# Kernel tuning notes

Hardware: AMD Instinct MI355X
Metric: run time of the kernel (lower is better)

The kernel has to match this reference:

```python
import jax, jax.numpy as jnp
import numpy as np

N = 30000   # fluid particles
E = 480000  # edges
F = 4       # fluidFeatures (in channels)
P = 8       # RBF basis size per dim (dims=[8], 1D)
LAYERS = [32, 64, 64, 2]


def hat_basis(x, n):
    # 'linear' RBF: hat functions on n evenly spaced centers in [-1, 1]
    centers = jnp.linspace(-1.0, 1.0, n, dtype=x.dtype)
    spacing = 2.0 / (n - 1)
    return jnp.maximum(0.0, 1.0 - jnp.abs(x[:, None] - centers[None, :]) / spacing)  # [E, n]


def rbf_conv(x, fi, fj, d, W, b, mask, n_nodes):
    # x: [N, Cin]; d: [E, 1] clamped; W: [P, Cin, Cout]; b: [Cout]
    phi = hat_basis(d[:, 0], W.shape[0])      # [E, P]
    xj = x[fj]                                 # gather source features [E, Cin]
    msg = jnp.zeros((xj.shape[0], W.shape[2]), dtype=x.dtype)
    for p in range(W.shape[0]):                # small fixed P=8 loop keeps memory O(E*Cout)
        msg = msg + phi[:, p, None] * (xj @ W[p])
    msg = jnp.where(mask[:, None], msg, 0.0)   # centerIgnore: drop self edges fi==fj
    out = jax.ops.segment_sum(msg, fi, num_segments=n_nodes)  # scatter-reduce to targets
    return out + b


def _xavier(key, shape_in, shape_out):
    lim = float(np.sqrt(6.0 / (shape_in + shape_out)))
    return jax.random.uniform(key, (shape_in, shape_out), jnp.float32, -lim, lim)


def setup_inputs() -> dict:
    key = jax.random.key(0)
    ks = jax.random.split(key, 16)
    fluidFeatures = jax.random.normal(ks[0], (N, F), jnp.float32)
    fi = jax.random.randint(ks[1], (E,), 0, N)
    fj = jax.random.randint(ks[2], (E,), 0, N)
    distances = jax.random.normal(ks[3], (E, 1), jnp.float32)
    # conv channels: 4->32, 64->64, 64->64, 64->2
    cio = [(F, 32), (2 * 32, 64), (64, 64), (64, 2)]
    inp = {"fluidFeatures": fluidFeatures, "fi": fi, "fj": fj, "distances": distances}
    for li, (ci, co) in enumerate(cio):
        inp[f"cW{li}"] = jax.random.normal(ks[4 + li], (P, ci, co), jnp.float32) * (1.0 / np.sqrt(P * ci))
        inp[f"cb{li}"] = jnp.zeros((co,), jnp.float32)
        inp[f"fW{li}"] = _xavier(ks[8 + li], ci, co)   # stored [in, out]
        inp[f"fb{li}"] = jnp.zeros((co,), jnp.float32)
    return inp


def reference(fluidFeatures, fi, fj, distances,
              cW0, cb0, fW0, fb0, cW1, cb1, fW1, fb1,
              cW2, cb2, fW2, fb2, cW3, cb3, fW3, fb3):
    n_nodes = fluidFeatures.shape[0]
    mask = fi != fj                     # centerIgnore (mask instead of filter: jit-safe)
    d = jnp.clip(distances, -1.0, 1.0)

    conv0 = rbf_conv(fluidFeatures, fi, fj, d, cW0, cb0, mask, n_nodes)  # [N, 32]
    lin0 = fluidFeatures @ fW0 + fb0                                      # [N, 32]
    ans = jnp.concatenate([lin0, conv0], axis=1)                          # [N, 64]

    # i = 1: features[0]=32 != features[1]=64 -> no residual
    ansc = jax.nn.relu(ans)
    ans = rbf_conv(ansc, fi, fj, d, cW1, cb1, mask, n_nodes) + (ansc @ fW1 + fb1)
    # i = 2: features[1]==features[2]==64 and shapes match -> residual
    ansc = jax.nn.relu(ans)
    ans = rbf_conv(ansc, fi, fj, d, cW2, cb2, mask, n_nodes) + (ansc @ fW2 + fb2) + ans
    # i = 3: 64 -> 2, no residual
    ansc = jax.nn.relu(ans)
    ans = rbf_conv(ansc, fi, fj, d, cW3, cb3, mask, n_nodes) + (ansc @ fW3 + fb3)

    return ans  # dim == 1 (dims=[8]) -> no /128
```

## Files before the change

kernel.cpp:

```cpp
#include <hip/hip_runtime.h>


#define CAP 48

typedef __attribute__((ext_vector_type(8))) short short8;
typedef __attribute__((ext_vector_type(4))) short short4v;
typedef __attribute__((ext_vector_type(4))) float f32x4;

__device__ __forceinline__ short bf16s(float f) {
  unsigned u = __float_as_uint(f);
  return (short)((u + 0x7FFF + ((u >> 16) & 1)) >> 16);
}
__device__ __forceinline__ float b2f(unsigned short s) {
  return __uint_as_float(((unsigned)s) << 16);
}

__global__ void fill_prep(const float* __restrict__ dist,
                          const int* __restrict__ fi, const int* __restrict__ fj,
                          int* __restrict__ cnt, int* __restrict__ jw, int nE,
                          const float* __restrict__ cW1, const float* __restrict__ fW1,
                          const float* __restrict__ cW2, const float* __restrict__ fW2,
                          short* __restrict__ wt1, short* __restrict__ wt2,
                          int fillBlocks) {
  if ((int)blockIdx.x < fillBlocks) {
    int e = blockIdx.x * blockDim.x + threadIdx.x;
    if (e >= nE) return;
    int i = fi[e], j = fj[e];
    if (i == j) return;
    float d = fminf(1.0f, fmaxf(-1.0f, dist[e]));
    float u = (d + 1.0f) * 3.5f;
    int p = min((int)u, 6);
    float w0 = 1.0f - (u - (float)p);
    int wq = (int)(w0 * 16383.0f + 0.5f);
    int pos = atomicAdd(&cnt[i], 1);
    if (pos < CAP)
      jw[(size_t)i * CAP + pos] = j | (p << 15) | (wq << 18);
  } else {
    int idx = ((int)blockIdx.x - fillBlocks) * blockDim.x + threadIdx.x;
    if (idx >= 2 * 576 * 64) return;
    int sel = idx / (576 * 64);
    int r = idx - sel * (576 * 64);
    int col = r >> 6, ch = r & 63;
    const float* cW = sel ? cW2 : cW1;
    const float* fW = sel ? fW2 : fW1;
    float v;
    if (col < 512) {
      int p = col >> 6, co = col & 63;
      v = cW[((size_t)p * 64 + ch) * 64 + co];
    } else {
      v = fW[(size_t)ch * 64 + (col - 512)];
    }
    (sel ? wt2 : wt1)[(size_t)col * 64 + ch] = bf16s(v);
  }
}

__global__ __launch_bounds__(256) void layer0_kernel(
    const float* __restrict__ X,
    const int* __restrict__ cnt, const int* __restrict__ jw,
    const float* __restrict__ cW0,
    const float* __restrict__ cb0,
    const float* __restrict__ fW0,
    const float* __restrict__ fb0,
    unsigned short* __restrict__ ansc0, int n) {
  __shared__ float sW[1024];
  __shared__ float sF[128];
  __shared__ float sB[64];
  __shared__ float sacc[4][32];
  for (int idx = threadIdx.x; idx < 1024; idx += 256) sW[idx] = cW0[idx];
  for (int idx = threadIdx.x; idx < 128; idx += 256) sF[idx] = fW0[idx];
  if (threadIdx.x < 32) sB[threadIdx.x] = cb0[threadIdx.x];
  else if (threadIdx.x < 64) sB[threadIdx.x] = fb0[threadIdx.x - 32];
  const int w = threadIdx.x >> 6;
  const int lane = threadIdx.x & 63;
  const int i = blockIdx.x * 4 + w;
  const bool valid = (i < n);
  if (valid && lane < 32) sacc[w][lane] = 0.0f;
  __syncthreads();
  if (valid && lane < min(cnt[i], CAP)) {
    int v = jw[(size_t)i * CAP + lane];
    int j = v & 0x7FFF;
    int p = (v >> 15) & 7;
    float w0 = (float)((unsigned)v >> 18) * (1.0f / 16383.0f);
    float w1 = 1.0f - w0;
    float4 x = *(const float4*)(X + (size_t)j * 4);
    atomicAdd(&sacc[w][p * 4 + 0], w0 * x.x);
    atomicAdd(&sacc[w][p * 4 + 1], w0 * x.y);
    atomicAdd(&sacc[w][p * 4 + 2], w0 * x.z);
    atomicAdd(&sacc[w][p * 4 + 3], w0 * x.w);
    atomicAdd(&sacc[w][(p + 1) * 4 + 0], w1 * x.x);
    atomicAdd(&sacc[w][(p + 1) * 4 + 1], w1 * x.y);
    atomicAdd(&sacc[w][(p + 1) * 4 + 2], w1 * x.z);
    atomicAdd(&sacc[w][(p + 1) * 4 + 3], w1 * x.w);
  }
  __syncthreads();
  if (!valid) return;
  const float4 xi = *(const float4*)(X + (size_t)i * 4);
  float v;
  if (lane < 32) {
    v = sB[32 + lane];
    v = fmaf(xi.x, sF[0 * 32 + lane], v);
    v = fmaf(xi.y, sF[1 * 32 + lane], v);
    v = fmaf(xi.z, sF[2 * 32 + lane], v);
    v = fmaf(xi.w, sF[3 * 32 + lane], v);
  } else {
    const int cc = lane - 32;
    v = sB[cc];
    #pragma unroll
    for (int k = 0; k < 32; ++k)
      v = fmaf(sacc[w][k], sW[k * 32 + cc], v);
  }
  ansc0[(size_t)i * 64 + lane] = (unsigned short)bf16s(fmaxf(v, 0.0f));
}

__global__ __launch_bounds__(256) void gemm_ul(
    const unsigned short* __restrict__ Xb,
    const short* __restrict__ WTul,
    unsigned short* __restrict__ UL, int n) {
  __shared__ short sUL[16 * 584];
  const int lane = threadIdx.x & 63;
  const int w = threadIdx.x >> 6;
  const int mrow = lane & 15;
  const int quad = lane >> 4;
  const int nodeBase = blockIdx.x * 16;
  const int bnode = min(nodeBase + mrow, n - 1);
  const unsigned short* bBase = Xb + (size_t)bnode * 64 + quad * 8;
  short8 b0 = *(const short8*)(bBase);
  short8 b1 = *(const short8*)(bBase + 32);
  #pragma unroll
  for (int t = 0; t < 9; ++t) {
    const int ct = w * 9 + t;
    const short* aBase = WTul + (size_t)(ct * 16 + mrow) * 64 + quad * 8;
    short8 a0 = *(const short8*)(aBase);
    short8 a1 = *(const short8*)(aBase + 32);
    f32x4 acc = {0, 0, 0, 0};
    acc = __builtin_amdgcn_mfma_f32_16x16x32_bf16(a0, b0, acc, 0, 0, 0);
    acc = __builtin_amdgcn_mfma_f32_16x16x32_bf16(a1, b1, acc, 0, 0, 0);
    short4v pk;
    #pragma unroll
    for (int reg = 0; reg < 4; ++reg) pk[reg] = bf16s(acc[reg]);
    *(short4v*)(sUL + mrow * 584 + ct * 16 + quad * 4) = pk;
  }
  __syncthreads();
  const int r = threadIdx.x >> 4;
  const int c0 = threadIdx.x & 15;
  if (nodeBase + r < n) {
    unsigned short* dst = UL + (size_t)(nodeBase + r) * 576;
    #pragma unroll
    for (int chunk = c0; chunk < 72; chunk += 16)
      *(short8*)(dst + chunk * 8) = *(const short8*)(sUL + r * 584 + chunk * 8);
  }
}

template <bool HAS_RES, bool STORE_ANS, bool COMPUTE_T>
__global__ __launch_bounds__(256) void conv_gather(
    const unsigned short* __restrict__ UL,
    const int* __restrict__ cnt, const int* __restrict__ jw,
    const float* __restrict__ cb, const float* __restrict__ fb,
    const float* __restrict__ resid,
    const float* __restrict__ cW3,
    float* __restrict__ T,
    float* __restrict__ outAns,
    unsigned short* __restrict__ outAnsc, int n) {
  const int lane = threadIdx.x & 63;
  const int half = lane >> 5;
  const int pl = lane & 31;
  const int i = (blockIdx.x * blockDim.x + threadIdx.x) >> 6;
  if (i >= n) return;
  int rec = jw[(size_t)i * CAP + (lane < CAP ? lane : 0)];
  const int m = min(cnt[i], CAP);
  const int mc = m - 1;
  const unsigned short* ULrow = UL + (size_t)i * 576;
  const unsigned Lraw = ((const unsigned*)(ULrow + 512))[pl];
  float rv0 = 0.0f, rv1 = 0.0f;
  if (HAS_RES) {
    float2 rv = *(const float2*)(resid + (size_t)i * 64 + 2 * pl);
    rv0 = rv.x; rv1 = rv.y;
  }
  float accLo = 0.0f, accHi = 0.0f;
  for (int q0 = 0; q0 < m; q0 += 16) {
    unsigned raw[16];
    float w0s[16];
    #pragma unroll
    for (int k = 0; k < 16; ++k) {
      int v = __builtin_amdgcn_readlane(rec, min(q0 + k, mc));
      int j = v & 0x7FFF;
      int p = (v >> 15) & 7;
      w0s[k] = (float)((unsigned)v >> 18) * (1.0f / 16383.0f);
      raw[k] = ((const unsigned*)(UL + (size_t)j * 576 + p * 64))[lane];
    }
    #pragma unroll
    for (int k = 0; k < 16; ++k) {
      bool ok = (q0 + k < m);
      float w = half ? (1.0f - w0s[k]) : w0s[k];
      w = ok ? w : 0.0f;
      accLo = fmaf(w, __uint_as_float(raw[k] << 16), accLo);
      accHi = fmaf(w, __uint_as_float(raw[k] & 0xFFFF0000u), accHi);
    }
  }
  accLo += __shfl_xor(accLo, 32, 64);
  accHi += __shfl_xor(accHi, 32, 64);
  if (half == 0) {
    const int c0i = 2 * pl, c1i = c0i + 1;
    float L0 = __uint_as_float(Lraw << 16);
    float L1 = __uint_as_float(Lraw & 0xFFFF0000u);
    float o0 = accLo + L0 + cb[c0i] + fb[c0i] + rv0;
    float o1 = accHi + L1 + cb[c1i] + fb[c1i] + rv1;
    if (STORE_ANS)
      *(float2*)(outAns + (size_t)i * 64 + c0i) = make_float2(o0, o1);
    unsigned short xb0 = (unsigned short)bf16s(fmaxf(o0, 0.0f));
    unsigned short xb1 = (unsigned short)bf16s(fmaxf(o1, 0.0f));
    ((unsigned*)(outAnsc + (size_t)i * 64))[pl] = (unsigned)xb0 | ((unsigned)xb1 << 16);
    if (COMPUTE_T) {
      float x0 = b2f(xb0), x1 = b2f(xb1);
      float c[16];
      #pragma unroll
      for (int t = 0; t < 16; ++t) {
        const float* wrow = cW3 + ((size_t)(t >> 1) * 64) * 2 + (t & 1);
        c[t] = x0 * wrow[c0i * 2] + x1 * wrow[c1i * 2];
      }
      #pragma unroll
      for (int off = 16; off > 0; off >>= 1) {
        #pragma unroll
        for (int t = 0; t < 16; ++t) c[t] += __shfl_xor(c[t], off, 64);
      }
      if (pl == 0) {
        float* tr = T + (size_t)i * 16;
        #pragma unroll
        for (int t = 0; t < 16; ++t) tr[t] = c[t];
      }
    }
  }
}

__global__ __launch_bounds__(256, 4) void layer3_kernel(
    const unsigned short* __restrict__ Xb,
    const float* __restrict__ T,
    const int* __restrict__ cnt, const int* __restrict__ jw,
    const float* __restrict__ cb3, const float* __restrict__ fb3,
    const float* __restrict__ fW3,
    float* __restrict__ out, int n) {
  const int lane = threadIdx.x & 63;
  const int i = (blockIdx.x * blockDim.x + threadIdx.x) >> 6;
  if (i >= n) return;
  const int m = min(cnt[i], CAP);
  float c0 = 0.0f, c1 = 0.0f;
  if (lane < m) {
    int v = jw[(size_t)i * CAP + lane];
    int j = min(v & 0x7FFF, n - 1);
    int p = (v >> 15) & 7;
    float w0 = (float)((unsigned)v >> 18) * (1.0f / 16383.0f);
    float w1 = 1.0f - w0;
    const float* tb = T + (size_t)j * 16 + p * 2;
    float2 ta = *(const float2*)(tb);
    float2 tc = *(const float2*)(tb + 2);
    c0 = w0 * ta.x + w1 * tc.x;
    c1 = w0 * ta.y + w1 * tc.y;
  }
  float xi = b2f(Xb[(size_t)i * 64 + lane]);
  float2 fw = *(const float2*)(fW3 + lane * 2);
  c0 = fmaf(xi, fw.x, c0);
  c1 = fmaf(xi, fw.y, c1);
  #pragma unroll
  for (int off = 32; off > 0; off >>= 1) {
    c0 += __shfl_xor(c0, off, 64);
    c1 += __shfl_xor(c1, off, 64);
  }
  if (lane == 0) {
    out[(size_t)i * 2 + 0] = c0 + cb3[0] + fb3[0];
    out[(size_t)i * 2 + 1] = c1 + cb3[1] + fb3[1];
  }
}

extern "C" void kernel_launch(void* const* d_in, const int* in_sizes, int n_in,
                              void* d_out, int out_size, void* d_ws, size_t ws_size,
                              hipStream_t stream) {
  const float* X    = (const float*)d_in[0];
  const int*   fi   = (const int*)d_in[1];
  const int*   fj   = (const int*)d_in[2];
  const float* dist = (const float*)d_in[3];
  const float* cW0 = (const float*)d_in[4];  const float* cb0 = (const float*)d_in[5];
  const float* fW0 = (const float*)d_in[6];  const float* fb0 = (const float*)d_in[7];
  const float* cW1 = (const float*)d_in[8];  const float* cb1 = (const float*)d_in[9];
  const float* fW1 = (const float*)d_in[10]; const float* fb1 = (const float*)d_in[11];
  const float* cW2 = (const float*)d_in[12]; const float* cb2 = (const float*)d_in[13];
  const float* fW2 = (const float*)d_in[14]; const float* fb2 = (const float*)d_in[15];
  const float* cW3 = (const float*)d_in[16]; const float* cb3 = (const float*)d_in[17];
  const float* fW3 = (const float*)d_in[18]; const float* fb3 = (const float*)d_in[19];
  float* out = (float*)d_out;

  const int n  = in_sizes[0] / 4;
  const int nE = in_sizes[1];

  unsigned short* UL    = (unsigned short*)d_ws;
  unsigned short* ansc0 = UL + (size_t)n * 576;
  unsigned short* ansc1 = ansc0 + (size_t)n * 64;
  float*          ans1  = (float*)(ansc1 + (size_t)n * 64);
  unsigned short* ansc2 = ansc0;
  float* T     = ans1 + (size_t)n * 64;
  short* wtul1 = (short*)(T + (size_t)n * 16);
  short* wtul2 = wtul1 + 576 * 64;
  int*   jw    = (int*)(wtul2 + 576 * 64);
  int*   cnt   = jw + (size_t)n * CAP;

  hipMemsetAsync(cnt, 0, (size_t)n * sizeof(int), stream);
  const int fillBlocks = (nE + 255) / 256;
  const int prepBlocks = (2 * 576 * 64 + 255) / 256;
  fill_prep<<<fillBlocks + prepBlocks, 256, 0, stream>>>(
      dist, fi, fj, cnt, jw, nE, cW1, fW1, cW2, fW2, wtul1, wtul2, fillBlocks);

  layer0_kernel<<<(n + 3) / 4, 256, 0, stream>>>(X, cnt, jw,
                                                 cW0, cb0, fW0, fb0, ansc0, n);
  gemm_ul<<<(n + 15) / 16, 256, 0, stream>>>(ansc0, wtul1, UL, n);
  conv_gather<false, true, false><<<(n * 64 + 255) / 256, 256, 0, stream>>>(
      UL, cnt, jw, cb1, fb1, nullptr, nullptr, nullptr, ans1, ansc1, n);
  gemm_ul<<<(n + 15) / 16, 256, 0, stream>>>(ansc1, wtul2, UL, n);
  conv_gather<true, false, true><<<(n * 64 + 255) / 256, 256, 0, stream>>>(
      UL, cnt, jw, cb2, fb2, ans1, cW3, T, nullptr, ansc2, n);
  layer3_kernel<<<(n * 64 + 255) / 256, 256, 0, stream>>>(ansc2, T, cnt, jw,
                                                          cb3, fb3, fW3, out, n);
}
```

Measured before the change: 269.3 us.

## Fuse layer-0 conv into the first UL GEMM kernel via shared memory

Merges the layer-0 gather/compute kernel with the following bf16 MFMA GEMM. Each block now handles 16 nodes, keeps the layer-0 activations in shared memory and feeds them straight into the MFMA, so the ansc0 buffer is never written to or re-read from global memory. This also removes one kernel launch. In exchange each block uses more shared memory and each wave handles four nodes' gathers, which may lower occupancy.

```diff
diff --git a/kernel.cpp b/kernel.cpp
--- a/kernel.cpp
+++ b/kernel.cpp
@@ -54,62 +54,122 @@
   }
 }
 
-__global__ __launch_bounds__(256) void layer0_kernel(
+__global__ __launch_bounds__(256) void layer0_gemm(
     const float* __restrict__ X,
     const int* __restrict__ cnt, const int* __restrict__ jw,
     const float* __restrict__ cW0,
     const float* __restrict__ cb0,
     const float* __restrict__ fW0,
     const float* __restrict__ fb0,
-    unsigned short* __restrict__ ansc0, int n) {
+    const short* __restrict__ WTul,
+    unsigned short* __restrict__ UL, int n) {
   __shared__ float sW[1024];
   __shared__ float sF[128];
   __shared__ float sB[64];
-  __shared__ float sacc[4][32];
+  __shared__ float sacc[16][32];
+  __shared__ __align__(16) unsigned short sXa[16 * 64];
+  __shared__ __align__(16) short sUL[16 * 584];
+  const int w = threadIdx.x >> 6;
+  const int lane = threadIdx.x & 63;
+  const int nodeBase = blockIdx.x * 16;
+
   for (int idx = threadIdx.x; idx < 1024; idx += 256) sW[idx] = cW0[idx];
   for (int idx = threadIdx.x; idx < 128; idx += 256) sF[idx] = fW0[idx];
   if (threadIdx.x < 32) sB[threadIdx.x] = cb0[threadIdx.x];
   else if (threadIdx.x < 64) sB[threadIdx.x] = fb0[threadIdx.x - 32];
-  const int w = threadIdx.x >> 6;
-  const int lane = threadIdx.x & 63;
-  const int i = blockIdx.x * 4 + w;
-  const bool valid = (i < n);
-  if (valid && lane < 32) sacc[w][lane] = 0.0f;
-  __syncthreads();
-  if (valid && lane < min(cnt[i], CAP)) {
-    int v = jw[(size_t)i * CAP + lane];
-    int j = v & 0x7FFF;
-    int p = (v >> 15) & 7;
-    float w0 = (float)((unsigned)v >> 18) * (1.0f / 16383.0f);
-    float w1 = 1.0f - w0;
-    float4 x = *(const float4*)(X + (size_t)j * 4);
-    atomicAdd(&sacc[w][p * 4 + 0], w0 * x.x);
-    atomicAdd(&sacc[w][p * 4 + 1], w0 * x.y);
-    atomicAdd(&sacc[w][p * 4 + 2], w0 * x.z);
-    atomicAdd(&sacc[w][p * 4 + 3], w0 * x.w);
-    atomicAdd(&sacc[w][(p + 1) * 4 + 0], w1 * x.x);
-    atomicAdd(&sacc[w][(p + 1) * 4 + 1], w1 * x.y);
-    atomicAdd(&sacc[w][(p + 1) * 4 + 2], w1 * x.z);
-    atomicAdd(&sacc[w][(p + 1) * 4 + 3], w1 * x.w);
-  }
-  __syncthreads();
-  if (!valid) return;
-  const float4 xi = *(const float4*)(X + (size_t)i * 4);
-  float v;
-  if (lane < 32) {
-    v = sB[32 + lane];
-    v = fmaf(xi.x, sF[0 * 32 + lane], v);
-    v = fmaf(xi.y, sF[1 * 32 + lane], v);
-    v = fmaf(xi.z, sF[2 * 32 + lane], v);
-    v = fmaf(xi.w, sF[3 * 32 + lane], v);
-  } else {
-    const int cc = lane - 32;
-    v = sB[cc];
-    #pragma unroll
-    for (int k = 0; k < 32; ++k)
-      v = fmaf(sacc[w][k], sW[k * 32 + cc], v);
-  }
-  ansc0[(size_t)i * 64 + lane] = (unsigned short)bf16s(fmaxf(v, 0.0f));
+  sacc[threadIdx.x >> 5][threadIdx.x & 31] = 0.0f;
+  sacc[8 + (threadIdx.x >> 5)][threadIdx.x & 31] = 0.0f;
+  __syncthreads();
+
+  const int slot = (lane < CAP) ? lane : 0;
+  int iN[4], mN[4], recN[4];
+  #pragma unroll
+  for (int s = 0; s < 4; ++s) {
+    iN[s] = nodeBase + w * 4 + s;
+    const bool v = iN[s] < n;
+    const int ic = v ? iN[s] : 0;
+    mN[s] = v ? min(cnt[ic], CAP) : 0;
+    recN[s] = jw[(size_t)ic * CAP + slot];
+  }
+  float4 xs[4];
+  #pragma unroll
+  for (int s = 0; s < 4; ++s) {
+    int j = min(recN[s] & 0x7FFF, n - 1);
+    xs[s] = *(const float4*)(X + (size_t)j * 4);
+  }
+  #pragma unroll
+  for (int s = 0; s < 4; ++s) {
+    if (lane < mN[s]) {
+      int v = recN[s];
+      int p = (v >> 15) & 7;
+      float w0 = (float)((unsigned)v >> 18) * (1.0f / 16383.0f);
+      float w1 = 1.0f - w0;
+      float* a = sacc[w * 4 + s];
+      atomicAdd(&a[p * 4 + 0], w0 * xs[s].x);
+      atomicAdd(&a[p * 4 + 1], w0 * xs[s].y);
+      atomicAdd(&a[p * 4 + 2], w0 * xs[s].z);
+      atomicAdd(&a[p * 4 + 3], w0 * xs[s].w);
+      atomicAdd(&a[(p + 1) * 4 + 0], w1 * xs[s].x);
+      atomicAdd(&a[(p + 1) * 4 + 1], w1 * xs[s].y);
+      atomicAdd(&a[(p + 1) * 4 + 2], w1 * xs[s].z);
+      atomicAdd(&a[(p + 1) * 4 + 3], w1 * xs[s].w);
+    }
+  }
+  __syncthreads();
+
+  #pragma unroll
+  for (int s = 0; s < 4; ++s) {
+    const int local = w * 4 + s;
+    const int i = iN[s];
+    float v = 0.0f;
+    if (i < n) {
+      const float4 xi = *(const float4*)(X + (size_t)i * 4);
+      if (lane < 32) {
+        v = sB[32 + lane];
+        v = fmaf(xi.x, sF[0 * 32 + lane], v);
+        v = fmaf(xi.y, sF[1 * 32 + lane], v);
+        v = fmaf(xi.z, sF[2 * 32 + lane], v);
+        v = fmaf(xi.w, sF[3 * 32 + lane], v);
+      } else {
+        const int cc = lane - 32;
+        v = sB[cc];
+        #pragma unroll
+        for (int k = 0; k < 32; ++k)
+          v = fmaf(sacc[local][k], sW[k * 32 + cc], v);
+      }
+      v = fmaxf(v, 0.0f);
+    }
+    sXa[local * 64 + lane] = (unsigned short)bf16s(v);
+  }
+  __syncthreads();
+
+  const int mrow = lane & 15;
+  const int quad = lane >> 4;
+  short8 b0 = *(const short8*)(sXa + mrow * 64 + quad * 8);
+  short8 b1 = *(const short8*)(sXa + mrow * 64 + quad * 8 + 32);
+  #pragma unroll
+  for (int t = 0; t < 9; ++t) {
+    const int ct = w * 9 + t;
+    const short* aBase = WTul + (size_t)(ct * 16 + mrow) * 64 + quad * 8;
+    short8 a0 = *(const short8*)(aBase);
+    short8 a1 = *(const short8*)(aBase + 32);
+    f32x4 acc = {0, 0, 0, 0};
+    acc = __builtin_amdgcn_mfma_f32_16x16x32_bf16(a0, b0, acc, 0, 0, 0);
+    acc = __builtin_amdgcn_mfma_f32_16x16x32_bf16(a1, b1, acc, 0, 0, 0);
+    short4v pk;
+    #pragma unroll
+    for (int reg = 0; reg < 4; ++reg) pk[reg] = bf16s(acc[reg]);
+    *(short4v*)(sUL + mrow * 584 + ct * 16 + quad * 4) = pk;
+  }
+  __syncthreads();
+  const int r = threadIdx.x >> 4;
+  const int c0 = threadIdx.x & 15;
+  if (nodeBase + r < n) {
+    unsigned short* dst = UL + (size_t)(nodeBase + r) * 576;
+    #pragma unroll
+    for (int chunk = c0; chunk < 72; chunk += 16)
+      *(short8*)(dst + chunk * 8) = *(const short8*)(sUL + r * 584 + chunk * 8);
+  }
 }
 
 __global__ __launch_bounds__(256) void gemm_ul(
@@ -292,10 +352,9 @@
   const int nE = in_sizes[1];
 
   unsigned short* UL    = (unsigned short*)d_ws;
-  unsigned short* ansc0 = UL + (size_t)n * 576;
-  unsigned short* ansc1 = ansc0 + (size_t)n * 64;
+  unsigned short* ansc2 = UL + (size_t)n * 576;
+  unsigned short* ansc1 = ansc2 + (size_t)n * 64;
   float*          ans1  = (float*)(ansc1 + (size_t)n * 64);
-  unsigned short* ansc2 = ansc0;
   float* T     = ans1 + (size_t)n * 64;
   short* wtul1 = (short*)(T + (size_t)n * 16);
   short* wtul2 = wtul1 + 576 * 64;
@@ -308,9 +367,8 @@
   fill_prep<<<fillBlocks + prepBlocks, 256, 0, stream>>>(
       dist, fi, fj, cnt, jw, nE, cW1, fW1, cW2, fW2, wtul1, wtul2, fillBlocks);
 
-  layer0_kernel<<<(n + 3) / 4, 256, 0, stream>>>(X, cnt, jw,
-                                                 cW0, cb0, fW0, fb0, ansc0, n);
-  gemm_ul<<<(n + 15) / 16, 256, 0, stream>>>(ansc0, wtul1, UL, n);
+  layer0_gemm<<<(n + 15) / 16, 256, 0, stream>>>(X, cnt, jw, cW0, cb0, fW0, fb0,
+                                                 wtul1, UL, n);
   conv_gather<false, true, false><<<(n * 64 + 255) / 256, 256, 0, stream>>>(
       UL, cnt, jw, cb1, fb1, nullptr, nullptr, nullptr, ans1, ansc1, n);
   gemm_ul<<<(n + 15) / 16, 256, 0, stream>>>(ansc1, wtul2, UL, n);
```

Result: faster. 256.3 us (-4.8%).
